# Optimization experiments

Hardware: AMD Instinct MI355X
Metric: run time of the kernel (lower is better)

## Reference

```python
import jax, jax.numpy as jnp
import numpy as np

B, C, N = 16, 3, 4096
K = 20
IN_CH, HID, OUT_CH = 2 * C, 64, 64
EPS = 1e-5
NEG_SLOPE = 0.2


def setup_inputs() -> dict:
    key = jax.random.key(0)
    ks = jax.random.split(key, 4)
    return {
        "x": jax.random.normal(ks[0], (B, C, N), dtype=jnp.float32),
        "W1": jax.random.normal(ks[1], (HID, IN_CH), dtype=jnp.float32) * 0.1,
        "W2": jax.random.normal(ks[2], (HID, HID), dtype=jnp.float32) * 0.1,
        "W3": jax.random.normal(ks[3], (OUT_CH, HID), dtype=jnp.float32) * 0.1,
        "g1": jnp.ones((HID,), jnp.float32),
        "b1": jnp.zeros((HID,), jnp.float32),
        "g2": jnp.ones((OUT_CH,), jnp.float32),
        "b2": jnp.zeros((OUT_CH,), jnp.float32),
    }


def _lrelu(y):
    return jnp.where(y > 0, y, NEG_SLOPE * y)


def _bn(y, gamma, beta):
    # training-mode BatchNorm2d: stats over all axes except channel (last here)
    mu = jnp.mean(y, axis=(0, 1, 2), keepdims=True)
    var = jnp.mean((y - mu) ** 2, axis=(0, 1, 2), keepdims=True)
    return (y - mu) * jax.lax.rsqrt(var + EPS) * gamma + beta


def _graph_feature(x, k):
    # x: [B, C, N] -> DGCNN edge features [B, N, k, 2C]
    xt = jnp.transpose(x, (0, 2, 1))  # [B, N, C]
    sq = jnp.sum(xt * xt, axis=-1)    # [B, N]
    # negative squared pairwise distance (top_k picks nearest, incl. self)
    neg_dist = 2.0 * jnp.einsum('bnc,bmc->bnm', xt, xt) - sq[:, :, None] - sq[:, None, :]
    _, idx = jax.lax.top_k(neg_dist, k)                 # [B, N, k]
    nbr = jax.vmap(lambda xb, ib: xb[ib])(xt, idx)      # [B, N, k, C] gather
    xc = jnp.broadcast_to(xt[:, :, None, :], nbr.shape)
    return jnp.concatenate([nbr - xc, xc], axis=-1)     # [B, N, k, 2C]


def reference(x, W1, W2, W3, g1, b1, g2, b2):
    f = _graph_feature(x, K)                    # [B, N, k, 2C]
    # 1x1 convs over channel axis (last), matching NCHW permute(0,3,2,1)
    y = jnp.einsum('bnkc,oc->bnko', f, W1)
    y = _bn(_lrelu(y), g1, b1)
    y = jnp.einsum('bnkc,oc->bnko', y, W2)
    y = _bn(_lrelu(y), g1, b1)                  # norm1 is reused (shared params)
    y = jnp.einsum('bnkc,oc->bnko', y, W3)
    y = _bn(_lrelu(y), g2, b2)
    y = jnp.max(y, axis=2)                      # max over k neighbors -> [B, N, out]
    return jnp.transpose(y, (0, 2, 1))          # [B, out, N]
```

## Files before the change

kernel.cpp:

```cpp
#include <hip/hip_runtime.h>
#include <math.h>

#define KNN 20
#define CNT_INV (1.0f / 1310720.0f)

typedef short bf16x8 __attribute__((ext_vector_type(8)));
typedef float f32x4  __attribute__((ext_vector_type(4)));

__device__ __forceinline__ short f2bf(float f) {
  unsigned u = __builtin_bit_cast(unsigned, f);
  u += 0x7FFFu + ((u >> 16) & 1u);
  return (short)(u >> 16);
}
__device__ __forceinline__ float lrelu(float y) { return y > 0.f ? y : 0.2f * y; }

__global__ __launch_bounds__(256) void xt4_kernel(const float* __restrict__ x,
                                                  float4* __restrict__ xt4) {
  const int t = blockIdx.x * 256 + threadIdx.x;
  const int b = t >> 12, m = t & 4095;
  const float* xb = x + (size_t)b * 12288;
  const float a = xb[m], c = xb[4096 + m], e = xb[8192 + m];
  xt4[t] = make_float4(a, c, e, a * a + c * c + e * e);
}

__global__ __launch_bounds__(256) void knn_kernel(const float4* __restrict__ xt4,
                                                  int* __restrict__ idx_out,
                                                  const float* __restrict__ W1,
                                                  float* __restrict__ s1buf) {
  __shared__ __align__(16) int hist[1024];
  __shared__ int sB[8];
  __shared__ int wcnt[4][4];
  __shared__ int slist[4][64];
  __shared__ int scnt[4];
  __shared__ int eidx[4][KNN];
  const int tid = threadIdx.x, lane = tid & 63, wid = tid >> 6;
  const int p0 = blockIdx.x * 4;
  const int b = p0 >> 12, n0 = p0 & 4095;
  const float4* xb4 = xt4 + (size_t)b * 4096;
  const float4 cp0 = xb4[n0], cp1 = xb4[n0 + 1], cp2 = xb4[n0 + 2], cp3 = xb4[n0 + 3];

  float w1r[6];
#pragma unroll
  for (int c = 0; c < 6; ++c) w1r[c] = W1[lane * 6 + c];

  float d0[16], d1[16], d2[16], d3[16];
#pragma unroll
  for (int i = 0; i < 16; ++i) {
    const float4 qv = xb4[i * 256 + tid];
    const float t0 = fmaf(cp0.x, qv.x, fmaf(cp0.y, qv.y, cp0.z * qv.z));
    const float t1 = fmaf(cp1.x, qv.x, fmaf(cp1.y, qv.y, cp1.z * qv.z));
    const float t2 = fmaf(cp2.x, qv.x, fmaf(cp2.y, qv.y, cp2.z * qv.z));
    const float t3 = fmaf(cp3.x, qv.x, fmaf(cp3.y, qv.y, cp3.z * qv.z));
    d0[i] = fmaxf(fmaf(-2.0f, t0, qv.w) + cp0.w, 0.0f);
    d1[i] = fmaxf(fmaf(-2.0f, t1, qv.w) + cp1.w, 0.0f);
    d2[i] = fmaxf(fmaf(-2.0f, t2, qv.w) + cp2.w, 0.0f);
    d3[i] = fmaxf(fmaf(-2.0f, t3, qv.w) + cp3.w, 0.0f);
  }

  float lo0 = 0.f, R0 = 1.f, lo1 = 0.f, R1 = 1.f, lo2 = 0.f, R2 = 1.f, lo3 = 0.f, R3 = 1.f;
  int bef0 = 0, bef1 = 0, bef2 = 0, bef3 = 0;
  float Dedge0 = 1e30f, Dedge1 = 1e30f, Dedge2 = 1e30f, Dedge3 = 1e30f;
  bool dn0 = false, dn1 = false, dn2 = false, dn3 = false;
  for (int pass = 0; pass < 6 && !(dn0 && dn1 && dn2 && dn3); ++pass) {
    *(int4*)&hist[tid * 4] = int4{0, 0, 0, 0};
    __syncthreads();
    const float sc0 = 256.0f / R0, sc1 = 256.0f / R1;
    const float sc2 = 256.0f / R2, sc3 = 256.0f / R3;
    if (!dn0) {
#pragma unroll
      for (int i = 0; i < 16; ++i) {
        const float rel = d0[i] - lo0;
        if (rel >= 0.0f && rel < R0) {
          int bin = (int)(rel * sc0); bin = bin > 255 ? 255 : bin;
          atomicAdd(&hist[bin], 1);
        }
      }
    }
    if (!dn1) {
#pragma unroll
      for (int i = 0; i < 16; ++i) {
        const float rel = d1[i] - lo1;
        if (rel >= 0.0f && rel < R1) {
          int bin = (int)(rel * sc1); bin = bin > 255 ? 255 : bin;
          atomicAdd(&hist[256 + bin], 1);
        }
      }
    }
    if (!dn2) {
#pragma unroll
      for (int i = 0; i < 16; ++i) {
        const float rel = d2[i] - lo2;
        if (rel >= 0.0f && rel < R2) {
          int bin = (int)(rel * sc2); bin = bin > 255 ? 255 : bin;
          atomicAdd(&hist[512 + bin], 1);
        }
      }
    }
    if (!dn3) {
#pragma unroll
      for (int i = 0; i < 16; ++i) {
        const float rel = d3[i] - lo3;
        if (rel >= 0.0f && rel < R3) {
          int bin = (int)(rel * sc3); bin = bin > 255 ? 255 : bin;
          atomicAdd(&hist[768 + bin], 1);
        }
      }
    }
    __syncthreads();
    {
      const bool skip = wid == 0 ? dn0 : wid == 1 ? dn1 : wid == 2 ? dn2 : dn3;
      if (!skip) {
        const int* h = &hist[wid * 256];
        int s0 = h[lane], s1 = h[64 + lane], s2 = h[128 + lane], s3 = h[192 + lane];
#pragma unroll
        for (int off = 1; off < 64; off <<= 1) { const int t = __shfl_up(s0, off); if (lane >= off) s0 += t; }
#pragma unroll
        for (int off = 1; off < 64; off <<= 1) { const int t = __shfl_up(s1, off); if (lane >= off) s1 += t; }
#pragma unroll
        for (int off = 1; off < 64; off <<= 1) { const int t = __shfl_up(s2, off); if (lane >= off) s2 += t; }
#pragma unroll
        for (int off = 1; off < 64; off <<= 1) { const int t = __shfl_up(s3, off); if (lane >= off) s3 += t; }
        s1 += __shfl(s0, 63);
        s2 += __shfl(s1, 63);
        s3 += __shfl(s2, 63);
        const int bef = wid == 0 ? bef0 : wid == 1 ? bef1 : wid == 2 ? bef2 : bef3;
        s0 += bef; s1 += bef; s2 += bef; s3 += bef;
        int B = 256, cnt = 0;
        unsigned long long m = __ballot(s0 >= 20);
        if (m) { const int l = __ffsll((long long)m) - 1; B = l; cnt = __shfl(s0, l); }
        else if ((m = __ballot(s1 >= 20)) != 0ull) { const int l = __ffsll((long long)m) - 1; B = 64 + l; cnt = __shfl(s1, l); }
        else if ((m = __ballot(s2 >= 20)) != 0ull) { const int l = __ffsll((long long)m) - 1; B = 128 + l; cnt = __shfl(s2, l); }
        else if ((m = __ballot(s3 >= 20)) != 0ull) { const int l = __ffsll((long long)m) - 1; B = 192 + l; cnt = __shfl(s3, l); }
        if (lane == 0) { sB[wid * 2] = B; sB[wid * 2 + 1] = cnt; }
      }
    }
    __syncthreads();
    bool zm0 = false, zm1 = false, zm2 = false, zm3 = false;
    if (!dn0) {
      const int Bq = sB[0], cq = sB[1];
      if (Bq == 256) R0 *= 16.0f;
      else {
        const float bw = R0 * (1.0f / 256.0f);
        Dedge0 = lo0 + (float)(Bq + 1) * bw;
        if (cq <= 48) dn0 = true;
        else { lo0 += (float)Bq * bw; R0 = bw; zm0 = true; }
      }
    }
    if (!dn1) {
      const int Bq = sB[2], cq = sB[3];
      if (Bq == 256) R1 *= 16.0f;
      else {
        const float bw = R1 * (1.0f / 256.0f);
        Dedge1 = lo1 + (float)(Bq + 1) * bw;
        if (cq <= 48) dn1 = true;
        else { lo1 += (float)Bq * bw; R1 = bw; zm1 = true; }
      }
    }
    if (!dn2) {
      const int Bq = sB[4], cq = sB[5];
      if (Bq == 256) R2 *= 16.0f;
      else {
        const float bw = R2 * (1.0f / 256.0f);
        Dedge2 = lo2 + (float)(Bq + 1) * bw;
        if (cq <= 48) dn2 = true;
        else { lo2 += (float)Bq * bw; R2 = bw; zm2 = true; }
      }
    }
    if (!dn3) {
      const int Bq = sB[6], cq = sB[7];
      if (Bq == 256) R3 *= 16.0f;
      else {
        const float bw = R3 * (1.0f / 256.0f);
        Dedge3 = lo3 + (float)(Bq + 1) * bw;
        if (cq <= 48) dn3 = true;
        else { lo3 += (float)Bq * bw; R3 = bw; zm3 = true; }
      }
    }
    if (zm0) {
      int c = 0;
#pragma unroll
      for (int i = 0; i < 16; ++i) c += (int)__popcll(__ballot(d0[i] < lo0));
      if (lane == 0) wcnt[0][wid] = c;
    }
    if (zm1) {
      int c = 0;
#pragma unroll
      for (int i = 0; i < 16; ++i) c += (int)__popcll(__ballot(d1[i] < lo1));
      if (lane == 0) wcnt[1][wid] = c;
    }
    if (zm2) {
      int c = 0;
#pragma unroll
      for (int i = 0; i < 16; ++i) c += (int)__popcll(__ballot(d2[i] < lo2));
      if (lane == 0) wcnt[2][wid] = c;
    }
    if (zm3) {
      int c = 0;
#pragma unroll
      for (int i = 0; i < 16; ++i) c += (int)__popcll(__ballot(d3[i] < lo3));
      if (lane == 0) wcnt[3][wid] = c;
    }
    if (zm0 | zm1 | zm2 | zm3) {
      __syncthreads();
      if (zm0) bef0 = wcnt[0][0] + wcnt[0][1] + wcnt[0][2] + wcnt[0][3];
      if (zm1) bef1 = wcnt[1][0] + wcnt[1][1] + wcnt[1][2] + wcnt[1][3];
      if (zm2) bef2 = wcnt[2][0] + wcnt[2][1] + wcnt[2][2] + wcnt[2][3];
      if (zm3) bef3 = wcnt[3][0] + wcnt[3][1] + wcnt[3][2] + wcnt[3][3];
    }
  }

  if (tid < 4) scnt[tid] = 0;
  __syncthreads();
  const float T0 = Dedge0 + 4e-3f, T1 = Dedge1 + 4e-3f;
  const float T2 = Dedge2 + 4e-3f, T3 = Dedge3 + 4e-3f;
#pragma unroll
  for (int i = 0; i < 16; ++i) {
    if (d0[i] < T0) {
      const int pos = atomicAdd(&scnt[0], 1);
      if (pos < 64) slist[0][pos] = i * 256 + tid;
    }
    if (d1[i] < T1) {
      const int pos = atomicAdd(&scnt[1], 1);
      if (pos < 64) slist[1][pos] = i * 256 + tid;
    }
    if (d2[i] < T2) {
      const int pos = atomicAdd(&scnt[2], 1);
      if (pos < 64) slist[2][pos] = i * 256 + tid;
    }
    if (d3[i] < T3) {
      const int pos = atomicAdd(&scnt[3], 1);
      if (pos < 64) slist[3][pos] = i * 256 + tid;
    }
  }
  __syncthreads();

  const float4 cp = wid == 0 ? cp0 : wid == 1 ? cp1 : wid == 2 ? cp2 : cp3;
  {
    const int s = min(scnt[wid], 64);
    int myi = -1; double myd = -1.0e300;
    if (lane < s) {
      myi = slist[wid][lane];
      const float4 av = xb4[myi];
      const double c0 = (double)cp.x, c1 = (double)cp.y, c2 = (double)cp.z;
      const double a0 = (double)av.x, a1 = (double)av.y, a2 = (double)av.z;
      const double dot = c0 * a0 + c1 * a1 + c2 * a2;
      const double sqm = a0 * a0 + a1 * a1 + a2 * a2;
      const double sn  = c0 * c0 + c1 * c1 + c2 * c2;
      myd = (2.0 * dot - sn) - sqm;
    }
    int rank = 0;
    for (int j = 0; j < s; ++j) {
      const double od = __shfl(myd, j);
      const int    oi = __shfl(myi, j);
      if (od > myd || (od == myd && oi < myi)) ++rank;
    }
    if (lane < s && rank < KNN) {
      idx_out[(p0 + wid) * KNN + rank] = myi;
      eidx[wid][rank] = myi;
    }
  }

  const float base1 = (w1r[3] - w1r[0]) * cp.x + (w1r[4] - w1r[1]) * cp.y +
                      (w1r[5] - w1r[2]) * cp.z;
  float sm = 0.f, sq = 0.f;
#pragma unroll
  for (int t = 0; t < KNN; ++t) {
    const int kk = eidx[wid][t];
    const float4 qv = xb4[kk];
    float y = fmaf(w1r[0], qv.x, fmaf(w1r[1], qv.y, fmaf(w1r[2], qv.z, base1)));
    y = lrelu(y);
    sm += y; sq = fmaf(y, y, sq);
  }
  float* bk = s1buf + (size_t)((p0 + wid) & 255) * 128;
  atomicAdd(&bk[lane], sm);
  atomicAdd(&bk[64 + lane], sq);
}

template <int STAGE, int MINW>
__global__ __launch_bounds__(256, MINW) void stage_kernel(
    const float4* __restrict__ xt4, const int* __restrict__ nbr,
    const float* __restrict__ W1,
    const float* __restrict__ w2ft, const float* __restrict__ b2f,
    const float* __restrict__ w3ft, const float* __restrict__ b3f,
    float* __restrict__ sumO, float* __restrict__ sqO,
    float* __restrict__ mx, float* __restrict__ mn) {
  __shared__ float pts[4][96];
  __shared__ float W1T[384];
  __shared__ short abuf[4][2048];
  __shared__ float redS[256], redQ[256];

  const int tid = threadIdx.x, wave = tid >> 6, lane = tid & 63;
  const int q = lane >> 4, cc = lane & 15;

  for (int i = tid; i < 384; i += 256) W1T[i] = W1[(i & 63) * 6 + (i >> 6)];
  __syncthreads();

  float w1r[6];
#pragma unroll
  for (int c = 0; c < 6; ++c) w1r[c] = W1T[c * 64 + lane];

  bf16x8 w2f[2][4];
#pragma unroll
  for (int kt = 0; kt < 2; ++kt)
#pragma unroll
    for (int nt = 0; nt < 4; ++nt)
#pragma unroll
      for (int j = 0; j < 8; ++j)
        w2f[kt][nt][j] = f2bf(w2ft[(kt * 32 + q * 8 + j) * 64 + nt * 16 + cc]);
  float bias2v[4];
#pragma unroll
  for (int nt = 0; nt < 4; ++nt) bias2v[nt] = b2f[nt * 16 + cc];

  bf16x8 w3f[2][4];
  float bias3v[4];
  if (STAGE == 3) {
#pragma unroll
    for (int kt = 0; kt < 2; ++kt)
#pragma unroll
      for (int nt = 0; nt < 4; ++nt)
#pragma unroll
        for (int j = 0; j < 8; ++j)
          w3f[kt][nt][j] = f2bf(w3ft[(kt * 32 + q * 8 + j) * 64 + nt * 16 + cc]);
#pragma unroll
    for (int nt = 0; nt < 4; ++nt) bias3v[nt] = b3f[nt * 16 + cc];
  }

  const int kt1 = lane >> 5, q1 = (lane & 31) >> 3, j1 = lane & 7;
  short* ab = abuf[wave];
  const bf16x8* ab8 = (const bf16x8*)ab;
  float* pw = pts[wave];

  float s_s[4] = {0.f, 0.f, 0.f, 0.f}, s_q[4] = {0.f, 0.f, 0.f, 0.f};
  const int wgid = blockIdx.x * 4 + wave;

  const int stepN = 8192 * KNN;
  const int* nbp = nbr + (size_t)wgid * KNN + lane;
  const float4* xb0 = xt4 + (size_t)(wgid >> 12) * 4096;
  const int nn = wgid & 4095;
  int kkB = 0;
  float4 g;
  if (lane < KNN) {
    const int kkA = nbp[0];
    g = xb0[kkA];
    kkB = nbp[stepN];
  } else if (lane == KNN) {
    g = xb0[nn];
  }
  const int* nbp2 = nbp + 2 * stepN;
  const float4* xbn = xb0 + 8192;

  for (int it = 0; it < 8; ++it) {
    const int p = wgid + it * 8192;
    if (lane <= KNN) *(float4*)&pw[lane * 4] = g;
    float4 gn = g; int kkC = kkB;
    if (it < 7 && lane <= KNN) gn = (lane < KNN) ? xbn[kkB] : xbn[nn];
    if (it < 6 && lane < KNN) kkC = nbp2[0];

    const float cx0 = pw[80], cx1 = pw[81], cx2 = pw[82];
    const float base1 = (w1r[3] - w1r[0]) * cx0 + (w1r[4] - w1r[1]) * cx1 +
                        (w1r[5] - w1r[2]) * cx2;

#pragma unroll
    for (int k = 0; k < KNN; ++k) {
      const float4 pk = *(const float4*)&pw[k * 4];
      float y = fmaf(w1r[0], pk.x, fmaf(w1r[1], pk.y, fmaf(w1r[2], pk.z, base1)));
      y = lrelu(y);
      ab[(((k >> 4) * 2 + kt1) * 64 + q1 * 16 + (k & 15)) * 8 + j1] = f2bf(y);
    }

    f32x4 acc2[2][4];
#pragma unroll
    for (int mt = 0; mt < 2; ++mt)
#pragma unroll
      for (int nt = 0; nt < 4; ++nt)
        acc2[mt][nt] = f32x4{bias2v[nt], bias2v[nt], bias2v[nt], bias2v[nt]};
#pragma unroll
    for (int kt = 0; kt < 2; ++kt) {
      const bf16x8 a0 = ab8[(0 * 2 + kt) * 64 + lane];
      const bf16x8 a1 = ab8[(1 * 2 + kt) * 64 + lane];
#pragma unroll
      for (int nt = 0; nt < 4; ++nt) {
        acc2[0][nt] = __builtin_amdgcn_mfma_f32_16x16x32_bf16(a0, w2f[kt][nt], acc2[0][nt], 0, 0, 0);
        acc2[1][nt] = __builtin_amdgcn_mfma_f32_16x16x32_bf16(a1, w2f[kt][nt], acc2[1][nt], 0, 0, 0);
      }
    }

    if (STAGE == 2) {
#pragma unroll
      for (int mt = 0; mt < 2; ++mt)
#pragma unroll
        for (int nt = 0; nt < 4; ++nt)
#pragma unroll
          for (int r = 0; r < 4; ++r) {
            if (mt == 1 && q != 0) continue;
            const float y = lrelu(acc2[mt][nt][r]);
            s_s[nt] += y; s_q[nt] += y * y;
          }
    } else {
#pragma unroll
      for (int mt = 0; mt < 2; ++mt)
#pragma unroll
        for (int nt = 0; nt < 4; ++nt) {
          const int kt3 = nt >> 1;
          const int q3 = (nt & 1) * 2 + (cc >> 3);
          const int j3 = cc & 7;
#pragma unroll
          for (int r = 0; r < 4; ++r) {
            if (mt == 1 && q != 0) continue;
            const float y = lrelu(acc2[mt][nt][r]);
            ab[((mt * 2 + kt3) * 64 + q3 * 16 + q * 4 + r) * 8 + j3] = f2bf(y);
          }
        }

      f32x4 acc3[2][4];
#pragma unroll
      for (int mt = 0; mt < 2; ++mt)
#pragma unroll
        for (int nt = 0; nt < 4; ++nt)
          acc3[mt][nt] = f32x4{bias3v[nt], bias3v[nt], bias3v[nt], bias3v[nt]};
#pragma unroll
      for (int kt = 0; kt < 2; ++kt) {
        const bf16x8 a0 = ab8[(0 * 2 + kt) * 64 + lane];
        const bf16x8 a1 = ab8[(1 * 2 + kt) * 64 + lane];
#pragma unroll
        for (int nt = 0; nt < 4; ++nt) {
          acc3[0][nt] = __builtin_amdgcn_mfma_f32_16x16x32_bf16(a0, w3f[kt][nt], acc3[0][nt], 0, 0, 0);
          acc3[1][nt] = __builtin_amdgcn_mfma_f32_16x16x32_bf16(a1, w3f[kt][nt], acc3[1][nt], 0, 0, 0);
        }
      }

      float vmx[4], vmn[4];
#pragma unroll
      for (int nt = 0; nt < 4; ++nt) { vmx[nt] = -INFINITY; vmn[nt] = INFINITY; }
#pragma unroll
      for (int mt = 0; mt < 2; ++mt)
#pragma unroll
        for (int nt = 0; nt < 4; ++nt)
#pragma unroll
          for (int r = 0; r < 4; ++r) {
            if (mt == 1 && q != 0) continue;
            const float y = lrelu(acc3[mt][nt][r]);
            s_s[nt] += y; s_q[nt] += y * y;
            vmx[nt] = fmaxf(vmx[nt], y); vmn[nt] = fminf(vmn[nt], y);
          }
#pragma unroll
      for (int nt = 0; nt < 4; ++nt) {
        vmx[nt] = fmaxf(vmx[nt], __shfl_xor(vmx[nt], 16));
        vmx[nt] = fmaxf(vmx[nt], __shfl_xor(vmx[nt], 32));
        vmn[nt] = fminf(vmn[nt], __shfl_xor(vmn[nt], 16));
        vmn[nt] = fminf(vmn[nt], __shfl_xor(vmn[nt], 32));
      }
      const float omx = q == 0 ? vmx[0] : q == 1 ? vmx[1] : q == 2 ? vmx[2] : vmx[3];
      const float omn = q == 0 ? vmn[0] : q == 1 ? vmn[1] : q == 2 ? vmn[2] : vmn[3];
      mx[(size_t)p * 64 + lane] = omx;
      mn[(size_t)p * 64 + lane] = omn;
    }

    g = gn; kkB = kkC; nbp2 += stepN; xbn += 8192;
  }

#pragma unroll
  for (int nt = 0; nt < 4; ++nt) {
    s_s[nt] += __shfl_xor(s_s[nt], 16); s_s[nt] += __shfl_xor(s_s[nt], 32);
    s_q[nt] += __shfl_xor(s_q[nt], 16); s_q[nt] += __shfl_xor(s_q[nt], 32);
  }
  const float ms = q == 0 ? s_s[0] : q == 1 ? s_s[1] : q == 2 ? s_s[2] : s_s[3];
  const float mq = q == 0 ? s_q[0] : q == 1 ? s_q[1] : q == 2 ? s_q[2] : s_q[3];
  redS[tid] = ms; redQ[tid] = mq;
  __syncthreads();
  if (tid < 64) {
    const float s  = redS[tid] + redS[64 + tid] + redS[128 + tid] + redS[192 + tid];
    const float qq = redQ[tid] + redQ[64 + tid] + redQ[128 + tid] + redQ[192 + tid];
    atomicAdd(&sumO[tid], s);
    atomicAdd(&sqO[tid], qq);
  }
}

__global__ void fold1_kernel(const float* __restrict__ s1buf,
                             const float* __restrict__ g, const float* __restrict__ bt,
                             const float* __restrict__ W,
                             float* __restrict__ WfT, float* __restrict__ bf) {
  __shared__ float s[64], t[64];
  const int o = threadIdx.x;
  float sm = 0.f, qq = 0.f;
  for (int k = 0; k < 256; ++k) { sm += s1buf[k * 128 + o]; qq += s1buf[k * 128 + 64 + o]; }
  const float mu = sm * CNT_INV;
  const float var = qq * CNT_INV - mu * mu;
  const float sc = g[o] / sqrtf(var + 1e-5f);
  s[o] = sc; t[o] = bt[o] - mu * sc;
  __syncthreads();
  float acc = 0.f;
  for (int c = 0; c < 64; ++c) {
    const float w = W[o * 64 + c];
    WfT[c * 64 + o] = w * s[c];
    acc += w * t[c];
  }
  bf[o] = acc;
}

__global__ void fold_kernel(const float* __restrict__ sum, const float* __restrict__ sq,
                            const float* __restrict__ g, const float* __restrict__ bt,
                            const float* __restrict__ W,
                            float* __restrict__ WfT, float* __restrict__ bf) {
  __shared__ float s[64], t[64];
  const int o = threadIdx.x;
  const float mu = sum[o] * CNT_INV;
  const float var = sq[o] * CNT_INV - mu * mu;
  const float sc = g[o] / sqrtf(var + 1e-5f);
  s[o] = sc; t[o] = bt[o] - mu * sc;
  __syncthreads();
  float acc = 0.f;
  for (int c = 0; c < 64; ++c) {
    const float w = W[o * 64 + c];
    WfT[c * 64 + o] = w * s[c];
    acc += w * t[c];
  }
  bf[o] = acc;
}

__global__ void fold3_kernel(const float* __restrict__ sum, const float* __restrict__ sq,
                             const float* __restrict__ g, const float* __restrict__ bt,
                             float* __restrict__ s3, float* __restrict__ t3) {
  const int o = threadIdx.x;
  const float mu = sum[o] * CNT_INV;
  const float var = sq[o] * CNT_INV - mu * mu;
  const float sc = g[o] / sqrtf(var + 1e-5f);
  s3[o] = sc; t3[o] = bt[o] - mu * sc;
}

__global__ __launch_bounds__(256) void final_kernel(
    const float* __restrict__ mx, const float* __restrict__ mn,
    const float* __restrict__ s3, const float* __restrict__ t3,
    float* __restrict__ out) {
  __shared__ float tmx[64][65], tmn[64][65];
  __shared__ float ss[64], tt[64];
  const int tid = threadIdx.x;
  const int P = blockIdx.x * 64;
  const int b = P >> 12, nb = P & 4095;
  if (tid < 64) { ss[tid] = s3[tid]; tt[tid] = t3[tid]; }
#pragma unroll
  for (int r = 0; r < 16; ++r) {
    const int idx = r * 256 + tid;
    const int pl = idx >> 6, ch = idx & 63;
    const size_t src = ((size_t)(P + pl)) * 64 + ch;
    tmx[pl][ch] = mx[src];
    tmn[pl][ch] = mn[src];
  }
  __syncthreads();
  const int nl = tid & 63;
#pragma unroll
  for (int r = 0; r < 16; ++r) {
    const int o = (tid >> 6) + r * 4;
    const float sc = ss[o];
    const float v = sc >= 0.f ? tmx[nl][o] : tmn[nl][o];
    out[(size_t)b * 262144 + (size_t)o * 4096 + nb + nl] = sc * v + tt[o];
  }
}

extern "C" void kernel_launch(void* const* d_in, const int* in_sizes, int n_in,
                              void* d_out, int out_size, void* d_ws, size_t ws_size,
                              hipStream_t stream) {
  const float* x  = (const float*)d_in[0];
  const float* W1 = (const float*)d_in[1];
  const float* W2 = (const float*)d_in[2];
  const float* W3 = (const float*)d_in[3];
  const float* g1 = (const float*)d_in[4];
  const float* b1 = (const float*)d_in[5];
  const float* g2 = (const float*)d_in[6];
  const float* b2 = (const float*)d_in[7];
  float* out = (float*)d_out;

  char* ws = (char*)d_ws;
  float4* xt4 = (float4*)ws;
  int* idx = (int*)(ws + 1048576);
  float* F = (float*)(ws + 6291456);
  float* sum2 = F + 0,   * sq2 = F + 64;
  float* sum3 = F + 128, * sq3 = F + 192;
  float* s1buf = F + 256;
  float* W2fT = F + 33024;
  float* b2f  = F + 37120;
  float* W3fT = F + 37184;
  float* b3f  = F + 41280;
  float* s3   = F + 41344;
  float* t3   = F + 41408;
  float* mx = (float*)(ws + 6457344);
  float* mn = mx + (size_t)16 * 4096 * 64;

  hipMemsetAsync(F, 0, 33024 * sizeof(float), stream);

  xt4_kernel<<<256, 256, 0, stream>>>(x, xt4);
  knn_kernel<<<16384, 256, 0, stream>>>(xt4, idx, W1, s1buf);
  fold1_kernel<<<1, 64, 0, stream>>>(s1buf, g1, b1, W2, W2fT, b2f);
  stage_kernel<2, 3><<<2048, 256, 0, stream>>>(xt4, idx, W1, W2fT, b2f, nullptr,
                                               nullptr, sum2, sq2, nullptr, nullptr);
  fold_kernel<<<1, 64, 0, stream>>>(sum2, sq2, g1, b1, W3, W3fT, b3f);
  stage_kernel<3, 2><<<2048, 256, 0, stream>>>(xt4, idx, W1, W2fT, b2f, W3fT,
                                               b3f, sum3, sq3, mx, mn);
  fold3_kernel<<<1, 64, 0, stream>>>(sum3, sq3, g2, b2, s3, t3);
  final_kernel<<<1024, 256, 0, stream>>>(mx, mn, s3, t3, out);
}
```

Before: 533.1 us.

## Replace first kNN radix-select pass with fixed-range per-query histogram and wave scan

The first pass of the kNN threshold search now builds one 256-bin histogram per query point over a fixed distance range [0,2), using disjoint hist slices for the four queries. Each wave then prefix-scans its query's histogram with shuffles and a ballot to find the bin holding the 20th neighbour. This either finishes the query immediately or narrows it to one bin, counting the points below that bin with ballot popcounts. The aim is to cut the iterative refinement passes, their barriers and the contended shared-memory atomics. It assumes the fixed range suits the data distribution and falls back to a wider range otherwise. The clamp of distances at zero is removed, which changes handling of slightly negative rounding values.

```diff
diff --git a/kernel.cpp b/kernel.cpp
--- a/kernel.cpp
+++ b/kernel.cpp
@@ -51,17 +51,118 @@
     const float t1 = fmaf(cp1.x, qv.x, fmaf(cp1.y, qv.y, cp1.z * qv.z));
     const float t2 = fmaf(cp2.x, qv.x, fmaf(cp2.y, qv.y, cp2.z * qv.z));
     const float t3 = fmaf(cp3.x, qv.x, fmaf(cp3.y, qv.y, cp3.z * qv.z));
-    d0[i] = fmaxf(fmaf(-2.0f, t0, qv.w) + cp0.w, 0.0f);
-    d1[i] = fmaxf(fmaf(-2.0f, t1, qv.w) + cp1.w, 0.0f);
-    d2[i] = fmaxf(fmaf(-2.0f, t2, qv.w) + cp2.w, 0.0f);
-    d3[i] = fmaxf(fmaf(-2.0f, t3, qv.w) + cp3.w, 0.0f);
-  }
-
-  float lo0 = 0.f, R0 = 1.f, lo1 = 0.f, R1 = 1.f, lo2 = 0.f, R2 = 1.f, lo3 = 0.f, R3 = 1.f;
+    d0[i] = fmaf(-2.0f, t0, qv.w) + cp0.w;
+    d1[i] = fmaf(-2.0f, t1, qv.w) + cp1.w;
+    d2[i] = fmaf(-2.0f, t2, qv.w) + cp2.w;
+    d3[i] = fmaf(-2.0f, t3, qv.w) + cp3.w;
+  }
+
+  *(int4*)&hist[tid * 4] = int4{0, 0, 0, 0};
+  __syncthreads();
+#pragma unroll
+  for (int i = 0; i < 16; ++i) {
+    if (d0[i] < 2.0f) atomicAdd(&hist[      (int)(d0[i] * 128.0f)], 1);
+    if (d1[i] < 2.0f) atomicAdd(&hist[256 + (int)(d1[i] * 128.0f)], 1);
+    if (d2[i] < 2.0f) atomicAdd(&hist[512 + (int)(d2[i] * 128.0f)], 1);
+    if (d3[i] < 2.0f) atomicAdd(&hist[768 + (int)(d3[i] * 128.0f)], 1);
+  }
+  __syncthreads();
+  {
+    const int* h = &hist[wid * 256];
+    int Bv = 256, cntv = 0, seam = 0;
+#pragma unroll
+    for (int c = 0; c < 4; ++c) {
+      if (Bv == 256) {
+        int s = h[c * 64 + lane];
+#pragma unroll
+        for (int off = 1; off < 64; off <<= 1) { const int t = __shfl_up(s, off); if (lane >= off) s += t; }
+        s += seam;
+        const unsigned long long m = __ballot(s >= 20);
+        if (m) { const int l = __ffsll((long long)m) - 1; Bv = c * 64 + l; cntv = __shfl(s, l); }
+        else seam = __shfl(s, 63);
+      }
+    }
+    if (lane == 0) { sB[wid * 2] = Bv; sB[wid * 2 + 1] = cntv; }
+  }
+  __syncthreads();
+
+  float lo0 = 0.f, R0 = 2.f, lo1 = 0.f, R1 = 2.f, lo2 = 0.f, R2 = 2.f, lo3 = 0.f, R3 = 2.f;
   int bef0 = 0, bef1 = 0, bef2 = 0, bef3 = 0;
   float Dedge0 = 1e30f, Dedge1 = 1e30f, Dedge2 = 1e30f, Dedge3 = 1e30f;
   bool dn0 = false, dn1 = false, dn2 = false, dn3 = false;
-  for (int pass = 0; pass < 6 && !(dn0 && dn1 && dn2 && dn3); ++pass) {
+  {
+    const float bw = 2.0f * (1.0f / 256.0f);
+    bool zm0 = false, zm1 = false, zm2 = false, zm3 = false;
+    {
+      const int Bq = sB[0], cq = sB[1];
+      if (Bq == 256) R0 = 32.0f;
+      else {
+        Dedge0 = (float)(Bq + 1) * bw;
+        if (cq <= 48) dn0 = true;
+        else { lo0 = (float)Bq * bw; R0 = bw; zm0 = true; }
+      }
+    }
+    {
+      const int Bq = sB[2], cq = sB[3];
+      if (Bq == 256) R1 = 32.0f;
+      else {
+        Dedge1 = (float)(Bq + 1) * bw;
+        if (cq <= 48) dn1 = true;
+        else { lo1 = (float)Bq * bw; R1 = bw; zm1 = true; }
+      }
+    }
+    {
+      const int Bq = sB[4], cq = sB[5];
+      if (Bq == 256) R2 = 32.0f;
+      else {
+        Dedge2 = (float)(Bq + 1) * bw;
+        if (cq <= 48) dn2 = true;
+        else { lo2 = (float)Bq * bw; R2 = bw; zm2 = true; }
+      }
+    }
+    {
+      const int Bq = sB[6], cq = sB[7];
+      if (Bq == 256) R3 = 32.0f;
+      else {
+        Dedge3 = (float)(Bq + 1) * bw;
+        if (cq <= 48) dn3 = true;
+        else { lo3 = (float)Bq * bw; R3 = bw; zm3 = true; }
+      }
+    }
+    if (zm0) {
+      int c = 0;
+#pragma unroll
+      for (int i = 0; i < 16; ++i) c += (int)__popcll(__ballot(d0[i] < lo0));
+      if (lane == 0) wcnt[0][wid] = c;
+    }
+    if (zm1) {
+      int c = 0;
+#pragma unroll
+      for (int i = 0; i < 16; ++i) c += (int)__popcll(__ballot(d1[i] < lo1));
+      if (lane == 0) wcnt[1][wid] = c;
+    }
+    if (zm2) {
+      int c = 0;
+#pragma unroll
+      for (int i = 0; i < 16; ++i) c += (int)__popcll(__ballot(d2[i] < lo2));
+      if (lane == 0) wcnt[2][wid] = c;
+    }
+    if (zm3) {
+      int c = 0;
+#pragma unroll
+      for (int i = 0; i < 16; ++i) c += (int)__popcll(__ballot(d3[i] < lo3));
+      if (lane == 0) wcnt[3][wid] = c;
+    }
+    if (zm0 | zm1 | zm2 | zm3) {
+      __syncthreads();
+      if (zm0) bef0 = wcnt[0][0] + wcnt[0][1] + wcnt[0][2] + wcnt[0][3];
+      if (zm1) bef1 = wcnt[1][0] + wcnt[1][1] + wcnt[1][2] + wcnt[1][3];
+      if (zm2) bef2 = wcnt[2][0] + wcnt[2][1] + wcnt[2][2] + wcnt[2][3];
+      if (zm3) bef3 = wcnt[3][0] + wcnt[3][1] + wcnt[3][2] + wcnt[3][3];
+    }
+  }
+
+  for (int pass = 1; pass < 6 && !(dn0 && dn1 && dn2 && dn3); ++pass) {
     *(int4*)&hist[tid * 4] = int4{0, 0, 0, 0};
     __syncthreads();
     const float sc0 = 256.0f / R0, sc1 = 256.0f / R1;
```

After: 519.1 us. 2.6% less time.
